# Kernel tuning notes

Measured on AMD Instinct MI355X. Metric: run time of the kernel, lower is better.

## Reference

```python
import jax, jax.numpy as jnp
import numpy as np

N = 131072      # num nodes
T = 16          # tile (block) size, tile_rows == tile_cols
BR = N // T     # block rows = 8192
K = 8           # nonzero blocks per block-row
IN_F, HID, NCLS = 128, 256, 64
LN_EPS = 1e-5


def setup_inputs() -> dict:
    key = jax.random.key(0)
    ks = jax.random.split(key, 8)
    features = jax.random.normal(ks[0], (N, IN_F), dtype=jnp.float32)
    block_vals = jax.random.uniform(ks[1], (BR, K, T, T), dtype=jnp.float32) / (K * T)
    block_cols = jax.random.randint(ks[2], (BR, K), 0, BR, dtype=jnp.int32)
    W0 = jax.random.normal(ks[3], (IN_F, HID), dtype=jnp.float32) / np.sqrt(IN_F)
    W1 = jax.random.normal(ks[4], (HID, HID), dtype=jnp.float32) / np.sqrt(HID)
    W2 = jax.random.normal(ks[5], (HID, NCLS), dtype=jnp.float32) / np.sqrt(HID)
    return {
        "features": features,
        "block_vals": block_vals,
        "W0": W0, "b0": jnp.zeros((HID,), jnp.float32),
        "W1": W1, "b1": jnp.zeros((HID,), jnp.float32),
        "W2": W2, "b2": jnp.zeros((NCLS,), jnp.float32),
        "g0": jnp.ones((HID,), jnp.float32), "beta0": jnp.zeros((HID,), jnp.float32),
        "g1": jnp.ones((HID,), jnp.float32), "beta1": jnp.zeros((HID,), jnp.float32),
        "block_cols": block_cols,
    }


def bcsr_spmm(block_vals, block_cols, z):
    """Block-CSR sparse matmul: out = A @ z.
    block_vals: [BR, K, T, T], block_cols: [BR, K] (block-column ids), z: [N, F]."""
    f = z.shape[-1]
    zb = z.reshape(BR, T, f)[block_cols]          # gather column blocks -> [BR, K, T, F]
    out = jnp.einsum('bkrc,bkcf->brf', block_vals, zb)  # block GEMM + accumulate over K
    return out.reshape(N, f)


def layer_norm(x, g, b):
    mu = jnp.mean(x, axis=-1, keepdims=True)
    var = jnp.mean(jnp.square(x - mu), axis=-1, keepdims=True)
    return g * (x - mu) * jax.lax.rsqrt(var + LN_EPS) + b


def reference(features, block_vals, W0, b0, W1, b1, W2, b2,
              g0, beta0, g1, beta1, block_cols):
    # layer 0: h' = A @ (h W0) + b0 ; relu ; LayerNorm
    h = bcsr_spmm(block_vals, block_cols, features @ W0) + b0
    h = layer_norm(jax.nn.relu(h), g0, beta0)
    # layer 1
    h = bcsr_spmm(block_vals, block_cols, h @ W1) + b1
    h = layer_norm(jax.nn.relu(h), g1, beta1)
    # output layer (no activation/norm)
    h = bcsr_spmm(block_vals, block_cols, h @ W2) + b2
    return h
```

## Files before the change

### kernel.cpp

```cpp
#include <hip/hip_runtime.h>
#include <hip/hip_bf16.h>


typedef __bf16 bf16;
typedef bf16 bf16x8 __attribute__((ext_vector_type(8)));
typedef bf16 bf16x4 __attribute__((ext_vector_type(4)));
typedef float f32x4 __attribute__((ext_vector_type(4)));

#define N_NODES 131072
#define BRQ 8192
#define KNZ 8
#define IN_F 128
#define HID 256
#define NCLS 64

static __device__ __forceinline__ f32x4 mfma16(bf16x8 a, bf16x8 b, f32x4 c) {
  return __builtin_amdgcn_mfma_f32_16x16x32_bf16(a, b, c, 0, 0, 0);
}

static __device__ __forceinline__ bf16x8 load8(const bf16* p) {
  return *(const bf16x8*)p;
}
static __device__ __forceinline__ bf16x8 cvt8(f32x4 a0, f32x4 a1) {
  bf16x8 r;
  r[0] = (bf16)a0[0]; r[1] = (bf16)a0[1]; r[2] = (bf16)a0[2]; r[3] = (bf16)a0[3];
  r[4] = (bf16)a1[0]; r[5] = (bf16)a1[1]; r[6] = (bf16)a1[2]; r[7] = (bf16)a1[3];
  return r;
}
static __device__ __forceinline__ bf16x8 load8(const float* p) {
  f32x4 a0 = *(const f32x4*)p;
  f32x4 a1 = *(const f32x4*)(p + 4);
  return cvt8(a0, a1);
}

template<typename TA, int KIN, int FOUT, int GRID>
__global__ __launch_bounds__(256, 4) void gemm_lds(const TA* __restrict__ X,
                                                   const float* __restrict__ W,
                                                   bf16* __restrict__ Zbt) {
  constexpr int CG  = FOUT / 64;
  constexpr int KS  = KIN / 32;
  constexpr int WGR = GRID / CG;
  constexpr int RTS = WGR * 4;
  constexpr int NT  = BRQ / RTS;
  constexpr int LDW = KIN + 8;

  const int tid  = threadIdx.x;
  const int wave = tid >> 6;
  const int lane = tid & 63;
  const int l15  = lane & 15;
  const int quad = lane >> 4;
  const int cg   = blockIdx.x % CG;
  const int rg   = blockIdx.x / CG;
  const int rt0  = rg * 4 + wave;

  __shared__ bf16 WL[64 * LDW];

  for (int e = tid; e < 64 * KIN; e += 256) {
    int c = e & 63, k = e >> 6;
    WL[c * LDW + k] = (bf16)W[(long)k * FOUT + cg * 64 + c];
  }

  const TA* __restrict__ xbase = X + (long)l15 * KIN + quad * 8;

  bf16x8 aw[2][KS];
#pragma unroll
  for (int k = 0; k < KS; ++k)
    aw[0][k] = load8(xbase + (long)rt0 * (16 * KIN) + k * 32);

  __syncthreads();

#pragma unroll
  for (int it = 0; it < NT; ++it) {
    const int rt = rt0 + it * RTS;
    if (it + 1 < NT) {
      const long xoff = (long)(rt + RTS) * (16 * KIN);
#pragma unroll
      for (int k = 0; k < KS; ++k)
        aw[(it + 1) & 1][k] = load8(xbase + xoff + k * 32);
    }
    f32x4 acc[4] = {};
    unsigned lo = 0;
#pragma unroll
    for (int k = 0; k < KS; ++k) {
      asm volatile("" : "+v"(lo));
#pragma unroll
      for (int t = 0; t < 4; ++t) {
        bf16x8 wf = *(const bf16x8*)(WL + lo + (t * 16 + l15) * LDW + k * 32 + quad * 8);
        acc[t] = mfma16(aw[it & 1][k], wf, acc[t]);
      }
    }
#pragma unroll
    for (int t = 0; t < 4; ++t) {
      int col = cg * 64 + t * 16 + l15;
      bf16x4 v;
#pragma unroll
      for (int i = 0; i < 4; ++i) v[i] = (bf16)acc[t][i];
      *(bf16x4*)(Zbt + ((long)rt * FOUT + col) * 16 + quad * 4) = v;
    }
  }
}

__global__ __launch_bounds__(256) void spmm_ln(const float* __restrict__ Abv,
                                               const int*   __restrict__ Abc,
                                               const bf16*  __restrict__ Zbt,
                                               const float* __restrict__ bias,
                                               const float* __restrict__ gamma,
                                               const float* __restrict__ beta,
                                               bf16* __restrict__ H) {
  const int wave = threadIdx.x >> 6;
  const int lane = threadIdx.x & 63;
  const int l15  = lane & 15;
  const int quad = lane >> 4;
  const int b    = blockIdx.x * 2 + (wave >> 1);
  const int ch   = wave & 1;

  const int*   bc    = Abc + b * KNZ;
  const int    cst   = (quad & 1) * 8;
  const int    half  = quad >> 1;
  const float* abase = Abv + (long)b * (KNZ * 256) + l15 * 16 + cst;

  bf16x8 afr[4];
  long   zb[4];
#pragma unroll
  for (int kp = 0; kp < 4; ++kp) {
    int blk = 2 * kp + half;
    afr[kp] = load8(abase + blk * 256);
    zb[kp]  = (long)bc[blk] * (HID * 16) + cst;
  }
  bf16x8 bfr[4][8];
#pragma unroll
  for (int kp = 0; kp < 4; ++kp)
#pragma unroll
    for (int t = 0; t < 8; ++t) {
      int f = ch * 128 + t * 16 + l15;
      bfr[kp][t] = *(const bf16x8*)(Zbt + zb[kp] + f * 16);
    }

  f32x4 acc[8] = {};
#pragma unroll
  for (int kp = 0; kp < 4; ++kp)
#pragma unroll
    for (int t = 0; t < 8; ++t)
      acc[t] = mfma16(afr[kp], bfr[kp][t], acc[t]);

  float gv[8], bv[8];
#pragma unroll
  for (int t = 0; t < 8; ++t) {
    int f = ch * 128 + t * 16 + l15;
    gv[t] = gamma[f];
    bv[t] = beta[f];
  }
  float ps[4] = {0.f, 0.f, 0.f, 0.f}, pss[4] = {0.f, 0.f, 0.f, 0.f};
#pragma unroll
  for (int t = 0; t < 8; ++t) {
    float bi = bias[ch * 128 + t * 16 + l15];
#pragma unroll
    for (int i = 0; i < 4; ++i) {
      float v = acc[t][i] + bi;
      v = v > 0.f ? v : 0.f;
      acc[t][i] = v;
      ps[i] += v;
      pss[i] += v * v;
    }
  }
#pragma unroll
  for (int m = 1; m < 16; m <<= 1) {
#pragma unroll
    for (int i = 0; i < 4; ++i) {
      ps[i]  += __shfl_xor(ps[i], m, 64);
      pss[i] += __shfl_xor(pss[i], m, 64);
    }
  }
  __shared__ float S[4][16], SS[4][16];
  if (l15 == 0) {
#pragma unroll
    for (int i = 0; i < 4; ++i) {
      S[wave][quad * 4 + i]  = ps[i];
      SS[wave][quad * 4 + i] = pss[i];
    }
  }
  __syncthreads();
#pragma unroll
  for (int i = 0; i < 4; ++i) {
    int r = quad * 4 + i;
    float s    = S[wave][r] + S[wave ^ 1][r];
    float ss   = SS[wave][r] + SS[wave ^ 1][r];
    float mu   = s * (1.f / 256.f);
    float var  = ss * (1.f / 256.f) - mu * mu;
    float rstd = rsqrtf(var + 1e-5f);
    bf16* hrow = H + (long)(b * 16 + r) * HID;
#pragma unroll
    for (int t = 0; t < 8; ++t) {
      int f = ch * 128 + t * 16 + l15;
      float y = (acc[t][i] - mu) * rstd * gv[t] + bv[t];
      hrow[f] = (bf16)y;
    }
  }
}

__global__ __launch_bounds__(256) void spmm_out(const float* __restrict__ Abv,
                                                const int*   __restrict__ Abc,
                                                const bf16*  __restrict__ Zbt,
                                                const float* __restrict__ bias,
                                                float* __restrict__ out) {
  const int wave = threadIdx.x >> 6;
  const int b    = blockIdx.x * 4 + wave;
  const int lane = threadIdx.x & 63;
  const int l15  = lane & 15;
  const int quad = lane >> 4;

  const int*   bc    = Abc + b * KNZ;
  const int    cst   = (quad & 1) * 8;
  const int    half  = quad >> 1;
  const float* abase = Abv + (long)b * (KNZ * 256) + l15 * 16 + cst;

  bf16x8 afr[4];
  long   zb[4];
#pragma unroll
  for (int kp = 0; kp < 4; ++kp) {
    int blk = 2 * kp + half;
    afr[kp] = load8(abase + blk * 256);
    zb[kp]  = (long)bc[blk] * (NCLS * 16) + cst;
  }
  bf16x8 bfr[4][4];
#pragma unroll
  for (int kp = 0; kp < 4; ++kp)
#pragma unroll
    for (int t = 0; t < 4; ++t) {
      int f = t * 16 + l15;
      bfr[kp][t] = *(const bf16x8*)(Zbt + zb[kp] + f * 16);
    }

  f32x4 acc[4] = {};
#pragma unroll
  for (int kp = 0; kp < 4; ++kp)
#pragma unroll
    for (int t = 0; t < 4; ++t)
      acc[t] = mfma16(afr[kp], bfr[kp][t], acc[t]);

#pragma unroll
  for (int t = 0; t < 4; ++t) {
    int f = t * 16 + l15;
    float bi = bias[f];
#pragma unroll
    for (int i = 0; i < 4; ++i) {
      out[(long)(b * 16 + quad * 4 + i) * NCLS + f] = acc[t][i] + bi;
    }
  }
}

extern "C" void kernel_launch(void* const* d_in, const int* in_sizes, int n_in,
                              void* d_out, int out_size, void* d_ws, size_t ws_size,
                              hipStream_t stream) {
  const float* features = (const float*)d_in[0];
  const float* bvals    = (const float*)d_in[1];
  const float* W0       = (const float*)d_in[2];
  const float* b0v      = (const float*)d_in[3];
  const float* W1       = (const float*)d_in[4];
  const float* b1v      = (const float*)d_in[5];
  const float* W2       = (const float*)d_in[6];
  const float* b2v      = (const float*)d_in[7];
  const float* g0       = (const float*)d_in[8];
  const float* beta0    = (const float*)d_in[9];
  const float* g1       = (const float*)d_in[10];
  const float* beta1    = (const float*)d_in[11];
  const int*   bcols    = (const int*)d_in[12];
  float* outp = (float*)d_out;

  char* ws = (char*)d_ws;
  bf16* zbt0 = (bf16*)(ws + (64L << 20));
  bf16* h0   = (bf16*)ws;
  bf16* zbt1 = (bf16*)(ws + (64L << 20));
  bf16* h1   = (bf16*)ws;
  bf16* zbt2 = (bf16*)(ws + (64L << 20));

  gemm_lds<float, IN_F, HID, 1024><<<dim3(1024), dim3(256), 0, stream>>>(features, W0, zbt0);
  spmm_ln<<<dim3(BRQ / 2), dim3(256), 0, stream>>>(bvals, bcols, zbt0, b0v, g0, beta0, h0);
  gemm_lds<bf16, HID, HID, 1024><<<dim3(1024), dim3(256), 0, stream>>>(h0, W1, zbt1);
  spmm_ln<<<dim3(BRQ / 2), dim3(256), 0, stream>>>(bvals, bcols, zbt1, b1v, g1, beta1, h1);
  gemm_lds<bf16, HID, NCLS, 512><<<dim3(512), dim3(256), 0, stream>>>(h1, W2, zbt2);
  spmm_out<<<dim3(BRQ / 4), dim3(256), 0, stream>>>(bvals, bcols, zbt2, b2v, outp);
}
```

Before: 445.9 us.

## Fuse LayerNorm output with next-layer dense GEMM inside SpMM kernels

Each spmm+LayerNorm kernel now keeps its normalized 16-row tile in LDS and immediately multiplies it by the next layer's weight using MFMA, writing the next Z tile directly. This removes the separate gemm launches and the global round trip of the hidden activations H. The W1/W2 bf16 transposes are produced by extra blocks appended to the first GEMM kernel and staged in the output buffer. In exchange, weights are read from global/L2 per block instead of being staged in LDS, and LDS use per block grows.

```diff
diff --git a/kernel.cpp b/kernel.cpp
--- a/kernel.cpp
+++ b/kernel.cpp
@@ -33,10 +33,12 @@
   return cvt8(a0, a1);
 }
 
-template<typename TA, int KIN, int FOUT, int GRID>
-__global__ __launch_bounds__(256, 4) void gemm_lds(const TA* __restrict__ X,
-                                                   const float* __restrict__ W,
-                                                   bf16* __restrict__ Zbt) {
+__global__ __launch_bounds__(256, 4) void gemm0_prep(
+    const float* __restrict__ X, const float* __restrict__ W0,
+    bf16* __restrict__ Zbt, const float* __restrict__ W1,
+    const float* __restrict__ W2, bf16* __restrict__ w1t,
+    bf16* __restrict__ w2t) {
+  constexpr int KIN = IN_F, FOUT = HID, GRID = 1024;
   constexpr int CG  = FOUT / 64;
   constexpr int KS  = KIN / 32;
   constexpr int WGR = GRID / CG;
@@ -44,7 +46,22 @@
   constexpr int NT  = BRQ / RTS;
   constexpr int LDW = KIN + 8;
 
-  const int tid  = threadIdx.x;
+  __shared__ bf16 WL[64 * LDW];
+  const int tid = threadIdx.x;
+
+  if (blockIdx.x >= GRID) {
+    int idx = (blockIdx.x - GRID) * 256 + tid;
+    if (idx < HID * HID) {
+      int r = idx >> 8, c = idx & 255;
+      w1t[c * HID + r] = (bf16)W1[idx];
+    } else {
+      int j = idx - HID * HID;
+      int r = j >> 6, c = j & 63;
+      w2t[c * HID + r] = (bf16)W2[j];
+    }
+    return;
+  }
+
   const int wave = tid >> 6;
   const int lane = tid & 63;
   const int l15  = lane & 15;
@@ -53,14 +70,12 @@
   const int rg   = blockIdx.x / CG;
   const int rt0  = rg * 4 + wave;
 
-  __shared__ bf16 WL[64 * LDW];
-
   for (int e = tid; e < 64 * KIN; e += 256) {
     int c = e & 63, k = e >> 6;
-    WL[c * LDW + k] = (bf16)W[(long)k * FOUT + cg * 64 + c];
-  }
-
-  const TA* __restrict__ xbase = X + (long)l15 * KIN + quad * 8;
+    WL[c * LDW + k] = (bf16)W0[(long)k * FOUT + cg * 64 + c];
+  }
+
+  const float* __restrict__ xbase = X + (long)l15 * KIN + quad * 8;
 
   bf16x8 aw[2][KS];
 #pragma unroll
@@ -100,19 +115,26 @@
   }
 }
 
-__global__ __launch_bounds__(256) void spmm_ln(const float* __restrict__ Abv,
-                                               const int*   __restrict__ Abc,
-                                               const bf16*  __restrict__ Zbt,
-                                               const float* __restrict__ bias,
-                                               const float* __restrict__ gamma,
-                                               const float* __restrict__ beta,
-                                               bf16* __restrict__ H) {
+template<int F_OUT>
+__global__ __launch_bounds__(256) void spmm_ln_gemm(
+    const float* __restrict__ Abv, const int* __restrict__ Abc,
+    const bf16*  __restrict__ Zbt, const float* __restrict__ bias,
+    const float* __restrict__ gamma, const float* __restrict__ beta,
+    const bf16*  __restrict__ WT,
+    bf16* __restrict__ Zout) {
+  constexpr int TD  = F_OUT / 32;
+  constexpr int LHW = HID + 8;
+
   const int wave = threadIdx.x >> 6;
   const int lane = threadIdx.x & 63;
   const int l15  = lane & 15;
   const int quad = lane >> 4;
   const int b    = blockIdx.x * 2 + (wave >> 1);
   const int ch   = wave & 1;
+  const int pair = wave >> 1;
+
+  __shared__ bf16  HL[2][16 * LHW];
+  __shared__ float S[4][16], SS[4][16];
 
   const int*   bc    = Abc + b * KNZ;
   const int    cst   = (quad & 1) * 8;
@@ -171,7 +193,6 @@
       pss[i] += __shfl_xor(pss[i], m, 64);
     }
   }
-  __shared__ float S[4][16], SS[4][16];
   if (l15 == 0) {
 #pragma unroll
     for (int i = 0; i < 4; ++i) {
@@ -188,13 +209,36 @@
     float mu   = s * (1.f / 256.f);
     float var  = ss * (1.f / 256.f) - mu * mu;
     float rstd = rsqrtf(var + 1e-5f);
-    bf16* hrow = H + (long)(b * 16 + r) * HID;
+    bf16* hrow = &HL[pair][r * LHW];
 #pragma unroll
     for (int t = 0; t < 8; ++t) {
       int f = ch * 128 + t * 16 + l15;
       float y = (acc[t][i] - mu) * rstd * gv[t] + bv[t];
       hrow[f] = (bf16)y;
     }
+  }
+  __syncthreads();
+
+  const long  rb    = blockIdx.x * 2 + pair;
+  const bf16* wbase = WT + (long)(ch * (F_OUT / 2) + l15) * HID + quad * 8;
+
+  f32x4 dacc[TD] = {};
+#pragma unroll
+  for (int k = 0; k < 8; ++k) {
+    bf16x8 ha = *(const bf16x8*)&HL[pair][l15 * LHW + k * 32 + quad * 8];
+#pragma unroll
+    for (int t = 0; t < TD; ++t) {
+      bf16x8 wf = *(const bf16x8*)(wbase + t * (16 * HID) + k * 32);
+      dacc[t] = mfma16(ha, wf, dacc[t]);
+    }
+  }
+#pragma unroll
+  for (int t = 0; t < TD; ++t) {
+    int col = ch * (F_OUT / 2) + t * 16 + l15;
+    bf16x4 v;
+#pragma unroll
+    for (int i = 0; i < 4; ++i) v[i] = (bf16)dacc[t][i];
+    *(bf16x4*)(Zout + (rb * F_OUT + col) * 16 + quad * 4) = v;
   }
 }
 
@@ -269,15 +313,17 @@
 
   char* ws = (char*)d_ws;
   bf16* zbt0 = (bf16*)(ws + (64L << 20));
-  bf16* h0   = (bf16*)ws;
-  bf16* zbt1 = (bf16*)(ws + (64L << 20));
-  bf16* h1   = (bf16*)ws;
+  bf16* zbt1 = (bf16*)ws;
   bf16* zbt2 = (bf16*)(ws + (64L << 20));
 
-  gemm_lds<float, IN_F, HID, 1024><<<dim3(1024), dim3(256), 0, stream>>>(features, W0, zbt0);
-  spmm_ln<<<dim3(BRQ / 2), dim3(256), 0, stream>>>(bvals, bcols, zbt0, b0v, g0, beta0, h0);
-  gemm_lds<bf16, HID, HID, 1024><<<dim3(1024), dim3(256), 0, stream>>>(h0, W1, zbt1);
-  spmm_ln<<<dim3(BRQ / 2), dim3(256), 0, stream>>>(bvals, bcols, zbt1, b1v, g1, beta1, h1);
-  gemm_lds<bf16, HID, NCLS, 512><<<dim3(512), dim3(256), 0, stream>>>(h1, W2, zbt2);
+  bf16* w1t = (bf16*)d_out;
+  bf16* w2t = w1t + HID * HID;
+
+  gemm0_prep<<<dim3(1024 + 320), dim3(256), 0, stream>>>(
+      features, W0, zbt0, W1, W2, w1t, w2t);
+  spmm_ln_gemm<HID><<<dim3(BRQ / 2), dim3(256), 0, stream>>>(
+      bvals, bcols, zbt0, b0v, g0, beta0, w1t, zbt1);
+  spmm_ln_gemm<NCLS><<<dim3(BRQ / 2), dim3(256), 0, stream>>>(
+      bvals, bcols, zbt1, b1v, g1, beta1, w2t, zbt2);
   spmm_out<<<dim3(BRQ / 4), dim3(256), 0, stream>>>(bvals, bcols, zbt2, b2v, outp);
 }
```

Measured after the change: 456.0 us. 1.02x slower.

## Fuse all six stages into one persistent kernel with grid barriers

Applied to the files above, without the earlier changes.

Turns the three GEMM and three SpMM kernels into device functions and runs them in sequence inside one persistent kernel of 1024 workgroups. Stages are separated by a software grid barrier built on an atomic counter and generation word. The goal is to remove per-launch overhead and the idle gaps between the six kernels. In exchange, the SpMM stages run as grid-stride loops over fewer workgroups. All workgroups must be co-resident, or the barrier deadlocks. The barrier words sit in the last 64 bytes of the output buffer, which the final stage overwrites.

```diff
diff --git a/kernel.cpp b/kernel.cpp
--- a/kernel.cpp
+++ b/kernel.cpp
@@ -13,6 +13,7 @@
 #define IN_F 128
 #define HID 256
 #define NCLS 64
+#define NWG 1024
 
 static __device__ __forceinline__ f32x4 mfma16(bf16x8 a, bf16x8 b, f32x4 c) {
   return __builtin_amdgcn_mfma_f32_16x16x32_bf16(a, b, c, 0, 0, 0);
@@ -33,10 +34,31 @@
   return cvt8(a0, a1);
 }
 
+static __device__ __forceinline__ void grid_bar(unsigned* cnt, unsigned* gen) {
+  __syncthreads();
+  if (threadIdx.x == 0) {
+    __threadfence();
+    unsigned g = __hip_atomic_load(gen, __ATOMIC_RELAXED, __HIP_MEMORY_SCOPE_AGENT);
+    unsigned arrived =
+        __hip_atomic_fetch_add(cnt, 1u, __ATOMIC_ACQ_REL, __HIP_MEMORY_SCOPE_AGENT);
+    if (arrived == NWG - 1) {
+      __hip_atomic_store(cnt, 0u, __ATOMIC_RELAXED, __HIP_MEMORY_SCOPE_AGENT);
+      __hip_atomic_fetch_add(gen, 1u, __ATOMIC_RELEASE, __HIP_MEMORY_SCOPE_AGENT);
+    } else {
+      while (__hip_atomic_load(gen, __ATOMIC_ACQUIRE, __HIP_MEMORY_SCOPE_AGENT) == g)
+        __builtin_amdgcn_s_sleep(8);
+    }
+    __threadfence();
+  }
+  __syncthreads();
+}
+
 template<typename TA, int KIN, int FOUT, int GRID>
-__global__ __launch_bounds__(256, 4) void gemm_lds(const TA* __restrict__ X,
-                                                   const float* __restrict__ W,
-                                                   bf16* __restrict__ Zbt) {
+static __device__ __forceinline__ void gemm_body(int wgid, int tid,
+                                                 const TA* __restrict__ X,
+                                                 const float* __restrict__ W,
+                                                 bf16* __restrict__ Zbt,
+                                                 bf16* WL) {
   constexpr int CG  = FOUT / 64;
   constexpr int KS  = KIN / 32;
   constexpr int WGR = GRID / CG;
@@ -44,16 +66,13 @@
   constexpr int NT  = BRQ / RTS;
   constexpr int LDW = KIN + 8;
 
-  const int tid  = threadIdx.x;
   const int wave = tid >> 6;
   const int lane = tid & 63;
   const int l15  = lane & 15;
   const int quad = lane >> 4;
-  const int cg   = blockIdx.x % CG;
-  const int rg   = blockIdx.x / CG;
+  const int cg   = wgid % CG;
+  const int rg   = wgid / CG;
   const int rt0  = rg * 4 + wave;
-
-  __shared__ bf16 WL[64 * LDW];
 
   for (int e = tid; e < 64 * KIN; e += 256) {
     int c = e & 63, k = e >> 6;
@@ -98,20 +117,19 @@
       *(bf16x4*)(Zbt + ((long)rt * FOUT + col) * 16 + quad * 4) = v;
     }
   }
-}
-
-__global__ __launch_bounds__(256) void spmm_ln(const float* __restrict__ Abv,
-                                               const int*   __restrict__ Abc,
-                                               const bf16*  __restrict__ Zbt,
-                                               const float* __restrict__ bias,
-                                               const float* __restrict__ gamma,
-                                               const float* __restrict__ beta,
-                                               bf16* __restrict__ H) {
-  const int wave = threadIdx.x >> 6;
-  const int lane = threadIdx.x & 63;
+  __syncthreads();
+}
+
+static __device__ __forceinline__ void spmm_ln_body(int wgid, int tid,
+    const float* __restrict__ Abv, const int* __restrict__ Abc,
+    const bf16* __restrict__ Zbt, const float* __restrict__ bias,
+    const float* __restrict__ gamma, const float* __restrict__ beta,
+    bf16* __restrict__ H, float* S, float* SS) {
+  const int wave = tid >> 6;
+  const int lane = tid & 63;
   const int l15  = lane & 15;
   const int quad = lane >> 4;
-  const int b    = blockIdx.x * 2 + (wave >> 1);
+  const int b    = wgid * 2 + (wave >> 1);
   const int ch   = wave & 1;
 
   const int*   bc    = Abc + b * KNZ;
@@ -171,20 +189,19 @@
       pss[i] += __shfl_xor(pss[i], m, 64);
     }
   }
-  __shared__ float S[4][16], SS[4][16];
   if (l15 == 0) {
 #pragma unroll
     for (int i = 0; i < 4; ++i) {
-      S[wave][quad * 4 + i]  = ps[i];
-      SS[wave][quad * 4 + i] = pss[i];
+      S[wave * 16 + quad * 4 + i]  = ps[i];
+      SS[wave * 16 + quad * 4 + i] = pss[i];
     }
   }
   __syncthreads();
 #pragma unroll
   for (int i = 0; i < 4; ++i) {
     int r = quad * 4 + i;
-    float s    = S[wave][r] + S[wave ^ 1][r];
-    float ss   = SS[wave][r] + SS[wave ^ 1][r];
+    float s    = S[wave * 16 + r] + S[(wave ^ 1) * 16 + r];
+    float ss   = SS[wave * 16 + r] + SS[(wave ^ 1) * 16 + r];
     float mu   = s * (1.f / 256.f);
     float var  = ss * (1.f / 256.f) - mu * mu;
     float rstd = rsqrtf(var + 1e-5f);
@@ -196,16 +213,16 @@
       hrow[f] = (bf16)y;
     }
   }
-}
-
-__global__ __launch_bounds__(256) void spmm_out(const float* __restrict__ Abv,
-                                                const int*   __restrict__ Abc,
-                                                const bf16*  __restrict__ Zbt,
-                                                const float* __restrict__ bias,
-                                                float* __restrict__ out) {
-  const int wave = threadIdx.x >> 6;
-  const int b    = blockIdx.x * 4 + wave;
-  const int lane = threadIdx.x & 63;
+  __syncthreads();
+}
+
+static __device__ __forceinline__ void spmm_out_body(int wgid, int tid,
+    const float* __restrict__ Abv, const int* __restrict__ Abc,
+    const bf16* __restrict__ Zbt, const float* __restrict__ bias,
+    float* __restrict__ out) {
+  const int wave = tid >> 6;
+  const int b    = wgid * 4 + wave;
+  const int lane = tid & 63;
   const int l15  = lane & 15;
   const int quad = lane >> 4;
 
@@ -247,6 +264,43 @@
       out[(long)(b * 16 + quad * 4 + i) * NCLS + f] = acc[t][i] + bi;
     }
   }
+}
+
+__global__ __launch_bounds__(256, 4) void mega(
+    const float* __restrict__ features, const float* __restrict__ bvals,
+    const float* __restrict__ W0, const float* __restrict__ b0v,
+    const float* __restrict__ W1, const float* __restrict__ b1v,
+    const float* __restrict__ W2, const float* __restrict__ b2v,
+    const float* __restrict__ g0, const float* __restrict__ beta0,
+    const float* __restrict__ g1, const float* __restrict__ beta1,
+    const int* __restrict__ bcols,
+    bf16* zbt0, bf16* zbt1, bf16* zbt2, bf16* h0, bf16* h1,
+    float* outp, unsigned* bar) {
+  __shared__ __align__(16) char LB[33792];
+  bf16*  WL = (bf16*)LB;
+  float* S  = (float*)LB;
+  float* SS = (float*)(LB + 256);
+
+  unsigned* cnt = bar;
+  unsigned* gen = bar + 1;
+
+  const int wg  = blockIdx.x;
+  const int tid = threadIdx.x;
+
+  gemm_body<float, IN_F, HID, NWG>(wg, tid, features, W0, zbt0, WL);
+  grid_bar(cnt, gen);
+  for (int i = wg; i < BRQ / 2; i += NWG)
+    spmm_ln_body(i, tid, bvals, bcols, zbt0, b0v, g0, beta0, h0, S, SS);
+  grid_bar(cnt, gen);
+  gemm_body<bf16, HID, HID, NWG>(wg, tid, h0, W1, zbt1, WL);
+  grid_bar(cnt, gen);
+  for (int i = wg; i < BRQ / 2; i += NWG)
+    spmm_ln_body(i, tid, bvals, bcols, zbt1, b1v, g1, beta1, h1, S, SS);
+  grid_bar(cnt, gen);
+  gemm_body<bf16, HID, NCLS, NWG>(wg, tid, h1, W2, zbt2, WL);
+  grid_bar(cnt, gen);
+  for (int i = wg; i < BRQ / 4; i += NWG)
+    spmm_out_body(i, tid, bvals, bcols, zbt2, b2v, outp);
 }
 
 extern "C" void kernel_launch(void* const* d_in, const int* in_sizes, int n_in,
@@ -274,10 +328,11 @@
   bf16* h1   = (bf16*)ws;
   bf16* zbt2 = (bf16*)(ws + (64L << 20));
 
-  gemm_lds<float, IN_F, HID, 1024><<<dim3(1024), dim3(256), 0, stream>>>(features, W0, zbt0);
-  spmm_ln<<<dim3(BRQ / 2), dim3(256), 0, stream>>>(bvals, bcols, zbt0, b0v, g0, beta0, h0);
-  gemm_lds<bf16, HID, HID, 1024><<<dim3(1024), dim3(256), 0, stream>>>(h0, W1, zbt1);
-  spmm_ln<<<dim3(BRQ / 2), dim3(256), 0, stream>>>(bvals, bcols, zbt1, b1v, g1, beta1, h1);
-  gemm_lds<bf16, HID, NCLS, 512><<<dim3(512), dim3(256), 0, stream>>>(h1, W2, zbt2);
-  spmm_out<<<dim3(BRQ / 4), dim3(256), 0, stream>>>(bvals, bcols, zbt2, b2v, outp);
-}
+  const size_t out_bytes = (size_t)N_NODES * NCLS * sizeof(float);
+  unsigned* bar = (unsigned*)((char*)d_out + out_bytes - 64);
+  hipMemsetAsync((void*)bar, 0, 64, stream);
+
+  mega<<<dim3(NWG), dim3(256), 0, stream>>>(
+      features, bvals, W0, b0v, W1, b1v, W2, b2v, g0, beta0, g1, beta1,
+      bcols, zbt0, zbt1, zbt2, h0, h1, outp, bar);
+}
```

Result: slower. 1.757 ms (+294.1%).
